# Kernel tuning notes

Measured on AMD Instinct MI355X. Metric: run time of the kernel, lower is better.

## Reference

```python
import jax, jax.numpy as jnp
import numpy as np

NUM_HEADS = 8
CUTOFF = 10.0


def layer_norm(x, g, b):
    m = x.mean(-1, keepdims=True)
    v = x.var(-1, keepdims=True)
    return (x - m) * jax.lax.rsqrt(v + 1e-5) * g + b


def mha(h, mask, Wq, Wk, Wv, Wo):
    # masked multi-head self-attention over the edge set; mask: [E,E] bool
    E, D = h.shape
    hd = D // NUM_HEADS
    q = (h @ Wq).reshape(E, NUM_HEADS, hd)
    k = (h @ Wk).reshape(E, NUM_HEADS, hd)
    v = (h @ Wv).reshape(E, NUM_HEADS, hd)
    s = jnp.einsum('ihd,jhd->hij', q, k) / jnp.sqrt(jnp.asarray(hd, h.dtype))
    s = jnp.where(mask[None], s, jnp.asarray(-1e9, h.dtype))
    p = jax.nn.softmax(s, axis=-1)  # [H,E,E]
    out = jnp.einsum('hij,jhd->ihd', p, v).reshape(E, D)
    return out @ Wo, p.mean(0)


def setup_inputs() -> dict:
    D, L, R, E, N, NB = 128, 3, 64, 3072, 1024, 16
    key = jax.random.key(0)
    ks = jax.random.split(key, 32)
    f32 = jnp.float32

    def w(i, shape, scale):
        return (jax.random.normal(ks[i], shape) * scale).astype(f32)

    s = 1.0 / np.sqrt(D)
    return {
        'edge_features': w(0, (E, D), 1.0),
        'edge_coords': w(1, (E, 3), 1.0),
        'edge_index': jax.random.randint(ks[2], (2, E), 0, N),
        'node_coords': w(3, (N, 3), 5.0),  # spread so distances span [0, cutoff]
        'block_ids': jax.random.randint(ks[4], (N,), 0, NB),
        'Wq_a': w(5, (L, D, D), s), 'Wk_a': w(6, (L, D, D), s),
        'Wv_a': w(7, (L, D, D), s), 'Wo_a': w(8, (L, D, D), s),
        'Wq_e': w(9, (L, D, D), s), 'Wk_e': w(10, (L, D, D), s),
        'Wv_e': w(11, (L, D, D), s), 'Wo_e': w(12, (L, D, D), s),
        'W1': w(13, (L, D, 4 * D), s), 'b1': jnp.zeros((L, 4 * D), f32),
        'W2': w(14, (L, 4 * D, D), 1.0 / np.sqrt(4 * D)), 'b2': jnp.zeros((L, D), f32),
        'ln1_g': jnp.ones((L, D), f32), 'ln1_b': jnp.zeros((L, D), f32),
        'ln2_g': jnp.ones((L, D), f32), 'ln2_b': jnp.zeros((L, D), f32),
        'ln3_g': jnp.ones((L, D), f32), 'ln3_b': jnp.zeros((L, D), f32),
        'Wrbf': w(15, (L, R, D), 1.0 / np.sqrt(R)),
        'Wc': w(16, (L, D), s), 'bc': jnp.zeros((L,), f32),
    }


def reference(edge_features, edge_coords, edge_index, node_coords, block_ids,
              Wq_a, Wk_a, Wv_a, Wo_a, Wq_e, Wk_e, Wv_e, Wo_e,
              W1, b1, W2, b2, ln1_g, ln1_b, ln2_g, ln2_b, ln3_g, ln3_b,
              Wrbf, Wc, bc):
    E = edge_features.shape[0]
    src, dst = edge_index[0], edge_index[1]
    bs, bd = block_ids[src], block_ids[dst]

    # intra-block mask: both endpoint blocks match between the two edges
    intra = (bs[:, None] == bs[None, :]) & (bd[:, None] == bd[None, :])
    # inter-block mask: edges that share a node but cross blocks
    share = ((src[:, None] == src[None, :]) | (src[:, None] == dst[None, :]) |
             (dst[:, None] == src[None, :]) | (dst[:, None] == dst[None, :]))
    inter = share & ~intra
    eye = jnp.eye(E, dtype=bool)
    intra = intra | eye
    inter = inter | eye

    # radial basis embedding of edge length with cosine cutoff
    R = Wrbf.shape[1]
    d = jnp.linalg.norm(node_coords[dst] - node_coords[src], axis=-1)  # [E]
    centers = jnp.linspace(0.0, CUTOFF, R).astype(edge_features.dtype)
    width = CUTOFF / R
    fc = 0.5 * (jnp.cos(jnp.pi * jnp.clip(d / CUTOFF, 0.0, 1.0)) + 1.0)
    rbf = jnp.exp(-(((d[:, None] - centers[None, :]) / width) ** 2)) * fc[:, None]

    h, x = edge_features, edge_coords
    L = Wq_a.shape[0]
    for l in range(L):
        h = h + rbf @ Wrbf[l]
        a, p_intra = mha(h, intra, Wq_a[l], Wk_a[l], Wv_a[l], Wo_a[l])
        h = layer_norm(h + a, ln1_g[l], ln1_b[l])
        e, _ = mha(h, inter, Wq_e[l], Wk_e[l], Wv_e[l], Wo_e[l])
        h = layer_norm(h + e, ln2_g[l], ln2_b[l])
        f = jax.nn.silu(h @ W1[l] + b1[l]) @ W2[l] + b2[l]
        h = layer_norm(h + f, ln3_g[l], ln3_b[l])
        # equivariant coordinate update (linear combination of equivariant vecs)
        gate = jnp.tanh(h @ Wc[l] + bc[l])[:, None]  # [E,1]
        x = x + gate * (x - p_intra @ x)
    return h, x
```

## Files before the change

### kernel.cpp

```cpp
#include <hip/hip_runtime.h>
#include <hip/hip_bf16.h>

typedef unsigned short u16;
typedef unsigned long long u64;
typedef __attribute__((ext_vector_type(4))) float f32x4;
typedef __attribute__((ext_vector_type(8))) short bf16x8;

#define NE 3072
#define DM 128
#define NH 8
#define HD 16
#define NL 3
#define NR 64
#define FF 512
#define CUT 10.0f
#define CAP 96
#define GRID 192
#define BR 16
#define NCLS 256

#define PK_QKV_A 0
#define PK_WO_A  49152
#define PK_QKV_E 65536
#define PK_WO_E  114688
#define PK_W1    131072
#define PK_W2    196608
#define PK_WRBF  262144
#define PK_LAYER 270336

__device__ __forceinline__ short f2b(float f) {
    union { __hip_bfloat16 b; short s; } u;
    u.b = __float2bfloat16(f);
    return u.s;
}
__device__ __forceinline__ void ast64(u64* p, u64 v) {
    __hip_atomic_store(p, v, __ATOMIC_RELAXED, __HIP_MEMORY_SCOPE_AGENT);
}
__device__ __forceinline__ void astf(float* p, float v) {
    __hip_atomic_store(p, v, __ATOMIC_RELAXED, __HIP_MEMORY_SCOPE_AGENT);
}
__device__ __forceinline__ float bfx(u64 v, int i) {
    return __uint_as_float(((unsigned)(v >> (16 * i)) & 0xFFFFu) << 16);
}

template <int KT, int S>
__device__ __forceinline__ f32x4 tileAb(const short* As, const short* Bt, int l) {
    f32x4 acc = {0.f, 0.f, 0.f, 0.f};
#pragma unroll
    for (int kt = 0; kt < KT; kt++) {
        bf16x8 av = *(const bf16x8*)(As + (l & 15) * S + kt * 32 + 8 * (l >> 4));
        bf16x8 bv = *(const bf16x8*)(Bt + kt * 512 + l * 8);
        acc = __builtin_amdgcn_mfma_f32_16x16x32_bf16(av, bv, acc, 0, 0, 0);
    }
    return acc;
}

__device__ __forceinline__ void gbar(int* cnt, int target) {
    __syncthreads();
    if (threadIdx.x == 0) {
        __hip_atomic_fetch_add(cnt, 1, __ATOMIC_RELEASE, __HIP_MEMORY_SCOPE_AGENT);
        while (__hip_atomic_load(cnt, __ATOMIC_RELAXED, __HIP_MEMORY_SCOPE_AGENT) < target)
            __builtin_amdgcn_s_sleep(2);
        asm volatile("" ::: "memory");
    }
    __syncthreads();
}

struct WSrc { const float* W[11]; };

__global__ __launch_bounds__(256)
void pack_w(WSrc ws, short* __restrict__ dst) {
    int gid = blockIdx.x * 256 + threadIdx.x;
    if (gid >= NL * PK_LAYER) return;
    int layer = gid / PK_LAYER, e = gid % PK_LAYER;
    int kind, off, K, N;
    if (e < 49152)       { kind = e / 16384;            off = e % 16384;      K = 128; N = 128; }
    else if (e < 65536)  { kind = 3;                    off = e - 49152;      K = 128; N = 128; }
    else if (e < 114688) { kind = 4 + (e - 65536) / 16384; off = (e - 65536) % 16384; K = 128; N = 128; }
    else if (e < 131072) { kind = 7;                    off = e - 114688;     K = 128; N = 128; }
    else if (e < 196608) { kind = 8;                    off = e - 131072;     K = 128; N = 512; }
    else if (e < 262144) { kind = 9;                    off = e - 196608;     K = 512; N = 128; }
    else                 { kind = 10;                   off = e - 262144;     K = 64;  N = 128; }
    int i = off & 7, lane = (off >> 3) & 63, ft = off >> 9;
    int KT = K >> 5;
    int kt = ft % KT, nt = ft / KT;
    int n = nt * 16 + (lane & 15);
    int k = kt * 32 + 8 * (lane >> 4) + i;
    const float* W = ws.W[kind] + (size_t)layer * K * N;
    dst[gid] = f2b(W[k * N + n]);
}

__global__ void zero_hist(int* hist, int* barcnt) {
    hist[threadIdx.x] = 0;
    if (threadIdx.x == 0) *barcnt = 0;
}

__global__ __launch_bounds__(256)
void k_meta(const int* __restrict__ eidx, const int* __restrict__ bids,
            int4* __restrict__ meta, int* __restrict__ key, int* __restrict__ hist) {
    int e = blockIdx.x * 256 + threadIdx.x;
    if (e >= NE) return;
    int s = eidx[e], d = eidx[NE + e];
    int bs = bids[s], bd = bids[d];
    meta[e] = make_int4(s, d, bs, bd);
    int kk = bs * 16 + bd;
    key[e] = kk;
    atomicAdd(&hist[kk], 1);
}

__global__ __launch_bounds__(256)
void k_scan(const int* __restrict__ hist, int* __restrict__ cls_start,
            int* __restrict__ fill) {
    __shared__ int sh[NCLS];
    int t = threadIdx.x;
    sh[t] = hist[t];
    __syncthreads();
    for (int off = 1; off < NCLS; off <<= 1) {
        int v = (t >= off) ? sh[t - off] : 0;
        __syncthreads();
        sh[t] += v;
        __syncthreads();
    }
    cls_start[t + 1] = sh[t];
    if (t == 0) cls_start[0] = 0;
    fill[t] = sh[t] - hist[t];
}

__global__ __launch_bounds__(256)
void k_scatter(const int* __restrict__ key, int* __restrict__ fill,
               int* __restrict__ perm) {
    int e = blockIdx.x * 256 + threadIdx.x;
    if (e >= NE) return;
    int pos = atomicAdd(&fill[key[e]], 1);
    perm[pos] = e;
}

__global__ __launch_bounds__(64)
void prep2(const float* __restrict__ ef, const float* __restrict__ ec,
           const float* __restrict__ nc, const int* __restrict__ perm,
           const int4* __restrict__ metaO, int4* __restrict__ meta2,
           float* __restrict__ h, float* __restrict__ xv, float* __restrict__ rbf) {
    int p = blockIdx.x, lane = threadIdx.x;
    int e = perm[p];
    int4 me = metaO[e];
    if (lane == 0) meta2[p] = me;
    h[p * DM + lane]      = ef[e * DM + lane];
    h[p * DM + 64 + lane] = ef[e * DM + 64 + lane];
    if (lane < 4) xv[p * 4 + lane] = (lane < 3) ? ec[e * 3 + lane] : 0.f;
    float dx = nc[me.y * 3 + 0] - nc[me.x * 3 + 0];
    float dy = nc[me.y * 3 + 1] - nc[me.x * 3 + 1];
    float dz = nc[me.y * 3 + 2] - nc[me.x * 3 + 2];
    float dist = sqrtf(dx * dx + dy * dy + dz * dz);
    float t = fminf(fmaxf(dist / CUT, 0.f), 1.f);
    float fc = 0.5f * (cosf(3.14159265358979f * t) + 1.f);
    float width = CUT / NR;
    float center = (CUT * lane) / (NR - 1);
    float u = (dist - center) / width;
    rbf[p * NR + lane] = expf(-u * u) * fc;
}

__global__ __launch_bounds__(64)
void build_lists(const int4* __restrict__ meta2,
                 u16* __restrict__ idx_e, int* __restrict__ cnt_e) {
    __shared__ int ce;
    __shared__ u16 be[CAP];
    int i = blockIdx.x, lane = threadIdx.x;
    if (lane == 0) ce = 0;
    __syncthreads();
    int4 mi = meta2[i];
    for (int j = lane; j < NE; j += 64) {
        int4 mj = meta2[j];
        bool intra_b = (mi.z == mj.z) && (mi.w == mj.w);
        bool share = (mi.x == mj.x) || (mi.x == mj.y) ||
                     (mi.y == mj.x) || (mi.y == mj.y);
        bool oke = (share && !intra_b) || (i == j);
        if (oke) { int p = atomicAdd(&ce, 1); if (p < CAP) be[p] = (u16)j; }
    }
    __syncthreads();
    int ne_ = min(ce, CAP);
    if (lane == 0) cnt_e[i] = ne_;
    for (int p = lane; p < ne_; p += 64) idx_e[i * CAP + p] = be[p];
}

__device__ __forceinline__ void attn_intra(
    const short (&qsb)[BR][136], const u64* __restrict__ kvaL,
    const float* __restrict__ xr, const int4* __restrict__ meta2,
    const int* __restrict__ cls_start,
    short (&ob)[BR][136], float (&pxs)[NH][BR][3],
    int m0, int w, int l)
{
    int rowl = l >> 2, sub = l & 3, row = m0 + rowl;
    const u64* q64 = reinterpret_cast<const u64*>(&qsb[rowl][w * HD]);
    u64 qc[4];
#pragma unroll
    for (int t = 0; t < 4; t++) qc[t] = q64[t];
    int4 mr = meta2[row];
    int c = mr.z * 16 + mr.w;
    int nb0 = cls_start[c], nb1 = cls_start[c + 1];

    float m = -1e30f, li = 0.f;
    float acc[HD + 3];
#pragma unroll
    for (int d = 0; d < HD + 3; d++) acc[d] = 0.f;

    for (int p2 = nb0 + sub; p2 < nb1; p2 += 4) {
        const u64* kb = kvaL + ((size_t)w * NE + p2) * 8;
        u64 kc[4], vc[4];
#pragma unroll
        for (int t = 0; t < 4; t++) { kc[t] = kb[t]; vc[t] = kb[4 + t]; }
        float x0 = xr[p2 * 4], x1 = xr[p2 * 4 + 1], x2 = xr[p2 * 4 + 2];
        float s = 0.f;
#pragma unroll
        for (int t = 0; t < 4; t++)
#pragma unroll
            for (int i = 0; i < 4; i++) s += bfx(qc[t], i) * bfx(kc[t], i);
        s *= 0.25f;
        if (s > m) {
            float cr = __expf(m - s);
            m = s; li *= cr;
#pragma unroll
            for (int d = 0; d < HD + 3; d++) acc[d] *= cr;
        }
        float pw = __expf(s - m);
        li += pw;
#pragma unroll
        for (int t = 0; t < 4; t++)
#pragma unroll
            for (int i = 0; i < 4; i++) acc[t * 4 + i] += pw * bfx(vc[t], i);
        acc[HD] += pw * x0; acc[HD + 1] += pw * x1; acc[HD + 2] += pw * x2;
    }

    float mA = fmaxf(m, __shfl_xor(m, 1));
    mA = fmaxf(mA, __shfl_xor(mA, 2));
    float cf = __expf(m - mA);
    li *= cf;
#pragma unroll
    for (int d = 0; d < HD + 3; d++) acc[d] *= cf;
#pragma unroll
    for (int off = 1; off <= 2; off <<= 1) {
        li += __shfl_xor(li, off);
#pragma unroll
        for (int d = 0; d < HD + 3; d++) acc[d] += __shfl_xor(acc[d], off);
    }
    if (sub == 0) {
        float inv = 1.f / li;
#pragma unroll
        for (int d = 0; d < HD; d += 2) {
            unsigned loq = (u16)f2b(acc[d] * inv);
            unsigned hiq = (u16)f2b(acc[d + 1] * inv);
            *reinterpret_cast<unsigned*>(&ob[rowl][w * HD + d]) = loq | (hiq << 16);
        }
        pxs[w][rowl][0] = acc[HD] * inv;
        pxs[w][rowl][1] = acc[HD + 1] * inv;
        pxs[w][rowl][2] = acc[HD + 2] * inv;
    }
}

__device__ __forceinline__ void attn_inter(
    const short (&qsb)[BR][136], const u64* __restrict__ kveL,
    const u16* __restrict__ idx, const int* __restrict__ cnt,
    short (&ob)[BR][136], int m0, int w, int l)
{
    int rowl = l >> 2, sub = l & 3, row = m0 + rowl;
    const u64* q64 = reinterpret_cast<const u64*>(&qsb[rowl][w * HD]);
    u64 qc[4];
#pragma unroll
    for (int t = 0; t < 4; t++) qc[t] = q64[t];
    const u64* kvh = kveL + (size_t)w * NE * 8;
    int n = cnt[row];
    float m = -1e30f, li = 0.f;
    float acc[HD];
#pragma unroll
    for (int d = 0; d < HD; d++) acc[d] = 0.f;

    for (int p = sub; p < n; p += 4) {
        int j = idx[row * CAP + p];
        const u64* kb = kvh + (size_t)j * 8;
        u64 kc[4], vc[4];
#pragma unroll
        for (int t = 0; t < 4; t++) { kc[t] = kb[t]; vc[t] = kb[4 + t]; }
        float s = 0.f;
#pragma unroll
        for (int t = 0; t < 4; t++)
#pragma unroll
            for (int i = 0; i < 4; i++) s += bfx(qc[t], i) * bfx(kc[t], i);
        s *= 0.25f;
        if (s > m) {
            float cr = __expf(m - s);
            m = s; li *= cr;
#pragma unroll
            for (int d = 0; d < HD; d++) acc[d] *= cr;
        }
        float pw = __expf(s - m);
        li += pw;
#pragma unroll
        for (int t = 0; t < 4; t++)
#pragma unroll
            for (int i = 0; i < 4; i++) acc[t * 4 + i] += pw * bfx(vc[t], i);
    }

    float mA = fmaxf(m, __shfl_xor(m, 1));
    mA = fmaxf(mA, __shfl_xor(mA, 2));
    float cf = __expf(m - mA);
    li *= cf;
#pragma unroll
    for (int d = 0; d < HD; d++) acc[d] *= cf;
#pragma unroll
    for (int off = 1; off <= 2; off <<= 1) {
        li += __shfl_xor(li, off);
#pragma unroll
        for (int d = 0; d < HD; d++) acc[d] += __shfl_xor(acc[d], off);
    }
    if (sub == 0) {
        float inv = 1.f / li;
#pragma unroll
        for (int d = 0; d < HD; d += 2) {
            unsigned loq = (u16)f2b(acc[d] * inv);
            unsigned hiq = (u16)f2b(acc[d + 1] * inv);
            *reinterpret_cast<unsigned*>(&ob[rowl][w * HD + d]) = loq | (hiq << 16);
        }
    }
}

__device__ __forceinline__ void ln_rows(float (&zs)[BR][132], float (&hF)[BR][132],
                                        short* hB, const float* g, const float* b,
                                        int w, int l) {
#pragma unroll
    for (int rr = 0; rr < 2; rr++) {
        int r = 2 * w + rr;
        float z0 = zs[r][l], z1 = zs[r][64 + l];
        float s = z0 + z1;
#pragma unroll
        for (int off = 32; off; off >>= 1) s += __shfl_xor(s, off);
        float mean = s * (1.f / DM);
        float d0 = z0 - mean, d1 = z1 - mean;
        float vs = d0 * d0 + d1 * d1;
#pragma unroll
        for (int off = 32; off; off >>= 1) vs += __shfl_xor(vs, off);
        float inv = rsqrtf(vs * (1.f / DM) + 1e-5f);
        float h0 = d0 * inv * g[l] + b[l];
        float h1 = d1 * inv * g[64 + l] + b[64 + l];
        hF[r][l] = h0; hF[r][64 + l] = h1;
        hB[r * 136 + l] = f2b(h0);
        hB[r * 136 + 64 + l] = f2b(h1);
    }
}

__global__ __launch_bounds__(512, 4)
void mega_kernel(const float* __restrict__ h_init, const float* __restrict__ rbf_g,
                 const int4* __restrict__ meta2, const int* __restrict__ cls_start,
                 const int* __restrict__ perm,
                 const u16* __restrict__ idx_e, const int* __restrict__ cnt_e,
                 const short* __restrict__ pk,
                 const float* __restrict__ b1g, const float* __restrict__ b2g,
                 const float* __restrict__ ln1g, const float* __restrict__ ln1b,
                 const float* __restrict__ ln2g, const float* __restrict__ ln2b,
                 const float* __restrict__ ln3g, const float* __restrict__ ln3b,
                 const float* __restrict__ Wcg, const float* __restrict__ bcg,
                 short* __restrict__ kva, short* __restrict__ kve,
                 float* __restrict__ xv, int* __restrict__ barcnt,
                 float* __restrict__ outp)
{
    __shared__ float hL[BR][132];
    __shared__ float hn[BR][132];
    __shared__ float zs[BR][132];
    __shared__ short qsb[BR][136];
    __shared__ short hb[BR][136];
    __shared__ short hnb[BR][136];
    __shared__ short ob[BR][136];
    __shared__ short rbfb[BR][72];
    __shared__ short ub[BR][520];
    __shared__ float pxs[NH][BR][3];

    int tid = threadIdx.x, w = tid >> 6, l = tid & 63;
    int m0 = blockIdx.x * BR;
    int R4 = 4 * (l >> 4), c0 = l & 15;

    for (int i = tid; i < BR * 128; i += 512) hL[i >> 7][i & 127] = h_init[m0 * DM + i];
    for (int i = tid; i < BR * 64; i += 512) rbfb[i >> 6][i & 63] = f2b(rbf_g[m0 * NR + i]);
    __syncthreads();

    int ph = 0;
    for (int lay = 0; lay < NL; lay++) {
        const short* Lb = pk + (size_t)lay * PK_LAYER;
        const float* xr = xv + (size_t)lay * NE * 4;
        float* xw2 = xv + (size_t)(lay + 1) * NE * 4;
        u64* kvaL = reinterpret_cast<u64*>(kva) + (size_t)lay * NH * NE * 8;
        u64* kveL = reinterpret_cast<u64*>(kve) + (size_t)lay * NH * NE * 8;
        bool last = (lay == NL - 1);

        {
            f32x4 acc = tileAb<2, 72>(&rbfb[0][0], Lb + PK_WRBF + w * 1024, l);
#pragma unroll
            for (int r = 0; r < 4; r++) {
                float z = acc[r] + hL[R4 + r][w * 16 + c0];
                hn[R4 + r][w * 16 + c0] = z;
                hnb[R4 + r][w * 16 + c0] = f2b(z);
            }
        }
        __syncthreads();
        {
            f32x4 aq = tileAb<4, 136>(&hnb[0][0], Lb + PK_QKV_A + 0 * 16384 + w * 2048, l);
#pragma unroll
            for (int r = 0; r < 4; r++) qsb[R4 + r][w * 16 + c0] = f2b(aq[r]);
            f32x4 ak = tileAb<4, 136>(&hnb[0][0], Lb + PK_QKV_A + 1 * 16384 + w * 2048, l);
            f32x4 av = tileAb<4, 136>(&hnb[0][0], Lb + PK_QKV_A + 2 * 16384 + w * 2048, l);
#pragma unroll
            for (int r = 0; r < 4; r++) {
                ub[R4 + r][w * 16 + c0] = f2b(ak[r]);
                ub[R4 + r][128 + w * 16 + c0] = f2b(av[r]);
            }
            __syncthreads();
            for (int u = tid; u < BR * 64; u += 512) {
                int r = u >> 6, rest = u & 63, hh = rest >> 3, j = rest & 7;
                int so = (j < 4) ? (hh * 16 + j * 4) : (128 + hh * 16 + (j - 4) * 4);
                u64 val = *reinterpret_cast<const u64*>(&ub[r][so]);
                ast64(kvaL + ((size_t)hh * NE + m0 + r) * 8 + j, val);
            }
        }
        gbar(barcnt, GRID * (++ph));

        attn_intra(qsb, kvaL, xr, meta2, cls_start, ob, pxs, m0, w, l);
        __syncthreads();
        {
            f32x4 d = tileAb<4, 136>(&ob[0][0], Lb + PK_WO_A + w * 2048, l);
#pragma unroll
            for (int r = 0; r < 4; r++)
                zs[R4 + r][w * 16 + c0] = d[r] + hn[R4 + r][w * 16 + c0];
        }
        __syncthreads();
        ln_rows(zs, hL, &hb[0][0], ln1g + lay * DM, ln1b + lay * DM, w, l);
        __syncthreads();

        {
            f32x4 aq = tileAb<4, 136>(&hb[0][0], Lb + PK_QKV_E + 0 * 16384 + w * 2048, l);
#pragma unroll
            for (int r = 0; r < 4; r++) qsb[R4 + r][w * 16 + c0] = f2b(aq[r]);
            f32x4 ak = tileAb<4, 136>(&hb[0][0], Lb + PK_QKV_E + 1 * 16384 + w * 2048, l);
            f32x4 av = tileAb<4, 136>(&hb[0][0], Lb + PK_QKV_E + 2 * 16384 + w * 2048, l);
#pragma unroll
            for (int r = 0; r < 4; r++) {
                ub[R4 + r][w * 16 + c0] = f2b(ak[r]);
                ub[R4 + r][128 + w * 16 + c0] = f2b(av[r]);
            }
            __syncthreads();
            for (int u = tid; u < BR * 64; u += 512) {
                int r = u >> 6, rest = u & 63, hh = rest >> 3, j = rest & 7;
                int so = (j < 4) ? (hh * 16 + j * 4) : (128 + hh * 16 + (j - 4) * 4);
                u64 val = *reinterpret_cast<const u64*>(&ub[r][so]);
                ast64(kveL + ((size_t)hh * NE + m0 + r) * 8 + j, val);
            }
        }
        gbar(barcnt, GRID * (++ph));

        attn_inter(qsb, kveL, idx_e, cnt_e, ob, m0, w, l);
        __syncthreads();
        {
            f32x4 d = tileAb<4, 136>(&ob[0][0], Lb + PK_WO_E + w * 2048, l);
#pragma unroll
            for (int r = 0; r < 4; r++)
                zs[R4 + r][w * 16 + c0] = d[r] + hL[R4 + r][w * 16 + c0];
        }
        __syncthreads();
        ln_rows(zs, hL, &hb[0][0], ln2g + lay * DM, ln2b + lay * DM, w, l);
        __syncthreads();

#pragma unroll
        for (int j = 0; j < 4; j++) {
            int nt = w * 4 + j;
            f32x4 acc = tileAb<4, 136>(&hb[0][0], Lb + PK_W1 + nt * 2048, l);
#pragma unroll
            for (int r = 0; r < 4; r++) {
                int col = nt * 16 + c0;
                float xvv = acc[r] + b1g[lay * FF + col];
                xvv = xvv / (1.f + __expf(-xvv));
                ub[R4 + r][col] = f2b(xvv);
            }
        }
        __syncthreads();
        {
            f32x4 acc = tileAb<16, 520>(&ub[0][0], Lb + PK_W2 + w * 8192, l);
#pragma unroll
            for (int r = 0; r < 4; r++)
                zs[R4 + r][w * 16 + c0] = acc[r] + b2g[lay * DM + w * 16 + c0]
                                        + hL[R4 + r][w * 16 + c0];
        }
        __syncthreads();
        {
            const float* g3 = ln3g + lay * DM;
            const float* b3 = ln3b + lay * DM;
            const float* Wcl = Wcg + lay * DM;
            float bc0 = bcg[lay];
#pragma unroll
            for (int rr = 0; rr < 2; rr++) {
                int r = 2 * w + rr, row = m0 + r;
                int orow = perm[row];
                float z0 = zs[r][l], z1 = zs[r][64 + l];
                float s = z0 + z1;
#pragma unroll
                for (int off = 32; off; off >>= 1) s += __shfl_xor(s, off);
                float mean = s * (1.f / DM);
                float d0 = z0 - mean, d1 = z1 - mean;
                float vsum = d0 * d0 + d1 * d1;
#pragma unroll
                for (int off = 32; off; off >>= 1) vsum += __shfl_xor(vsum, off);
                float inv = rsqrtf(vsum * (1.f / DM) + 1e-5f);
                float h0 = d0 * inv * g3[l] + b3[l];
                float h1 = d1 * inv * g3[64 + l] + b3[64 + l];
                hL[r][l] = h0; hL[r][64 + l] = h1;
                if (last) { outp[orow * DM + l] = h0; outp[orow * DM + 64 + l] = h1; }
                float dc = h0 * Wcl[l] + h1 * Wcl[64 + l];
#pragma unroll
                for (int off = 32; off; off >>= 1) dc += __shfl_xor(dc, off);
                float gate = tanhf(dc + bc0);
                if (l < 3) {
                    float pxm = 0.f;
#pragma unroll
                    for (int hh = 0; hh < NH; hh++) pxm += pxs[hh][r][l];
                    pxm *= 0.125f;
                    float xvv = xr[row * 4 + l];
                    float nx = xvv + gate * (xvv - pxm);
                    astf(xw2 + row * 4 + l, nx);
                    if (last) outp[NE * DM + orow * 3 + l] = nx;
                }
            }
        }
        __syncthreads();
    }
}

extern "C" void kernel_launch(void* const* d_in, const int* in_sizes, int n_in,
                              void* d_out, int out_size, void* d_ws, size_t ws_size,
                              hipStream_t stream) {
    const float* ef   = (const float*)d_in[0];
    const float* ec   = (const float*)d_in[1];
    const int*   eidx = (const int*)d_in[2];
    const float* nc   = (const float*)d_in[3];
    const int*   bids = (const int*)d_in[4];
    const float* b1   = (const float*)d_in[14];
    const float* b2   = (const float*)d_in[16];
    const float* ln1g = (const float*)d_in[17];
    const float* ln1b = (const float*)d_in[18];
    const float* ln2g = (const float*)d_in[19];
    const float* ln2b = (const float*)d_in[20];
    const float* ln3g = (const float*)d_in[21];
    const float* ln3b = (const float*)d_in[22];
    const float* Wc   = (const float*)d_in[24];
    const float* bc   = (const float*)d_in[25];
    float* out = (float*)d_out;

    char* w = (char*)d_ws;
    auto carve = [&](size_t bytes) { char* p = w; w += ((bytes + 255) / 256) * 256; return p; };
    int*   barcnt = (int*)carve(256);
    int*   hist   = (int*)carve(NCLS * 4);
    int*   csta   = (int*)carve((NCLS + 1) * 4);
    int*   fill   = (int*)carve(NCLS * 4);
    int*   key    = (int*)carve((size_t)NE * 4);
    int*   perm   = (int*)carve((size_t)NE * 4);
    int4*  metaO  = (int4*)carve((size_t)NE * 16);
    int4*  meta2  = (int4*)carve((size_t)NE * 16);
    float* xv     = (float*)carve((size_t)(NL + 1) * NE * 4 * 4);
    int*   cnt_e  = (int*)carve((size_t)NE * 4);
    u16*   idx_e  = (u16*)carve((size_t)NE * CAP * 2);
    float* rbf_g  = (float*)carve((size_t)NE * NR * 4);
    float* h_in   = (float*)carve((size_t)NE * DM * 4);
    short* kva    = (short*)carve((size_t)NL * NH * NE * 32 * 2);
    short* kve    = (short*)carve((size_t)NL * NH * NE * 32 * 2);
    short* pk     = (short*)carve((size_t)NL * PK_LAYER * 2);

    WSrc ws;
    ws.W[0] = (const float*)d_in[5];   ws.W[1] = (const float*)d_in[6];
    ws.W[2] = (const float*)d_in[7];   ws.W[3] = (const float*)d_in[8];
    ws.W[4] = (const float*)d_in[9];   ws.W[5] = (const float*)d_in[10];
    ws.W[6] = (const float*)d_in[11];  ws.W[7] = (const float*)d_in[12];
    ws.W[8] = (const float*)d_in[13];  ws.W[9] = (const float*)d_in[15];
    ws.W[10] = (const float*)d_in[23];
    pack_w<<<(NL * PK_LAYER + 255) / 256, 256, 0, stream>>>(ws, pk);

    zero_hist<<<1, 256, 0, stream>>>(hist, barcnt);
    k_meta<<<(NE + 255) / 256, 256, 0, stream>>>(eidx, bids, metaO, key, hist);
    k_scan<<<1, 256, 0, stream>>>(hist, csta, fill);
    k_scatter<<<(NE + 255) / 256, 256, 0, stream>>>(key, fill, perm);
    prep2<<<NE, 64, 0, stream>>>(ef, ec, nc, perm, metaO, meta2, h_in, xv, rbf_g);
    build_lists<<<NE, 64, 0, stream>>>(meta2, idx_e, cnt_e);

    mega_kernel<<<GRID, 512, 0, stream>>>(h_in, rbf_g, meta2, csta, perm,
                                          idx_e, cnt_e, pk,
                                          b1, b2, ln1g, ln1b, ln2g, ln2b, ln3g, ln3b,
                                          Wc, bc, kva, kve, xv, barcnt, out);
}
```

Measured before the change: 171.9 us.

## Fuse setup kernels into one persistent kernel and prefetch K/V in attention loops

Merges weight packing, histogram, scan, scatter, per-edge prep and neighbor-list construction into a single persistent setup kernel that uses grid-wide atomic barriers, replacing seven launches with two. The histogram scan becomes a wave-level shuffle scan, and edge metadata is stored with a 64-byte stride. Both attention loops now software-prefetch the next K/V row and coordinates before computing on the current one. The grid barriers assume all 384 blocks are co-resident, and the prefetch raises register pressure in the mega kernel.

```diff
diff --git a/kernel.cpp b/kernel.cpp
--- a/kernel.cpp
+++ b/kernel.cpp
@@ -18,6 +18,8 @@
 #define GRID 192
 #define BR 16
 #define NCLS 256
+#define SB 384
+#define ST 512
 
 #define PK_QKV_A 0
 #define PK_WO_A  49152
@@ -39,6 +41,9 @@
 __device__ __forceinline__ void astf(float* p, float v) {
     __hip_atomic_store(p, v, __ATOMIC_RELAXED, __HIP_MEMORY_SCOPE_AGENT);
 }
+__device__ __forceinline__ int aldi(const int* p) {
+    return __hip_atomic_load(p, __ATOMIC_RELAXED, __HIP_MEMORY_SCOPE_AGENT);
+}
 __device__ __forceinline__ float bfx(u64 v, int i) {
     return __uint_as_float(((unsigned)(v >> (16 * i)) & 0xFFFFu) << 16);
 }
@@ -68,123 +73,129 @@
 
 struct WSrc { const float* W[11]; };
 
-__global__ __launch_bounds__(256)
-void pack_w(WSrc ws, short* __restrict__ dst) {
-    int gid = blockIdx.x * 256 + threadIdx.x;
-    if (gid >= NL * PK_LAYER) return;
-    int layer = gid / PK_LAYER, e = gid % PK_LAYER;
-    int kind, off, K, N;
-    if (e < 49152)       { kind = e / 16384;            off = e % 16384;      K = 128; N = 128; }
-    else if (e < 65536)  { kind = 3;                    off = e - 49152;      K = 128; N = 128; }
-    else if (e < 114688) { kind = 4 + (e - 65536) / 16384; off = (e - 65536) % 16384; K = 128; N = 128; }
-    else if (e < 131072) { kind = 7;                    off = e - 114688;     K = 128; N = 128; }
-    else if (e < 196608) { kind = 8;                    off = e - 131072;     K = 128; N = 512; }
-    else if (e < 262144) { kind = 9;                    off = e - 196608;     K = 512; N = 128; }
-    else                 { kind = 10;                   off = e - 262144;     K = 64;  N = 128; }
-    int i = off & 7, lane = (off >> 3) & 63, ft = off >> 9;
-    int KT = K >> 5;
-    int kt = ft % KT, nt = ft / KT;
-    int n = nt * 16 + (lane & 15);
-    int k = kt * 32 + 8 * (lane >> 4) + i;
-    const float* W = ws.W[kind] + (size_t)layer * K * N;
-    dst[gid] = f2b(W[k * N + n]);
-}
-
-__global__ void zero_hist(int* hist, int* barcnt) {
-    hist[threadIdx.x] = 0;
-    if (threadIdx.x == 0) *barcnt = 0;
-}
-
-__global__ __launch_bounds__(256)
-void k_meta(const int* __restrict__ eidx, const int* __restrict__ bids,
-            int4* __restrict__ meta, int* __restrict__ key, int* __restrict__ hist) {
-    int e = blockIdx.x * 256 + threadIdx.x;
-    if (e >= NE) return;
-    int s = eidx[e], d = eidx[NE + e];
-    int bs = bids[s], bd = bids[d];
-    meta[e] = make_int4(s, d, bs, bd);
-    int kk = bs * 16 + bd;
-    key[e] = kk;
-    atomicAdd(&hist[kk], 1);
-}
-
-__global__ __launch_bounds__(256)
-void k_scan(const int* __restrict__ hist, int* __restrict__ cls_start,
-            int* __restrict__ fill) {
-    __shared__ int sh[NCLS];
+__global__ void zeroK(int* hist, int* barA, int* barM) {
     int t = threadIdx.x;
-    sh[t] = hist[t];
-    __syncthreads();
-    for (int off = 1; off < NCLS; off <<= 1) {
-        int v = (t >= off) ? sh[t - off] : 0;
-        __syncthreads();
-        sh[t] += v;
-        __syncthreads();
-    }
-    cls_start[t + 1] = sh[t];
-    if (t == 0) cls_start[0] = 0;
-    fill[t] = sh[t] - hist[t];
-}
-
-__global__ __launch_bounds__(256)
-void k_scatter(const int* __restrict__ key, int* __restrict__ fill,
-               int* __restrict__ perm) {
-    int e = blockIdx.x * 256 + threadIdx.x;
-    if (e >= NE) return;
-    int pos = atomicAdd(&fill[key[e]], 1);
-    perm[pos] = e;
-}
-
-__global__ __launch_bounds__(64)
-void prep2(const float* __restrict__ ef, const float* __restrict__ ec,
-           const float* __restrict__ nc, const int* __restrict__ perm,
-           const int4* __restrict__ metaO, int4* __restrict__ meta2,
-           float* __restrict__ h, float* __restrict__ xv, float* __restrict__ rbf) {
-    int p = blockIdx.x, lane = threadIdx.x;
-    int e = perm[p];
-    int4 me = metaO[e];
-    if (lane == 0) meta2[p] = me;
-    h[p * DM + lane]      = ef[e * DM + lane];
-    h[p * DM + 64 + lane] = ef[e * DM + 64 + lane];
-    if (lane < 4) xv[p * 4 + lane] = (lane < 3) ? ec[e * 3 + lane] : 0.f;
-    float dx = nc[me.y * 3 + 0] - nc[me.x * 3 + 0];
-    float dy = nc[me.y * 3 + 1] - nc[me.x * 3 + 1];
-    float dz = nc[me.y * 3 + 2] - nc[me.x * 3 + 2];
-    float dist = sqrtf(dx * dx + dy * dy + dz * dz);
-    float t = fminf(fmaxf(dist / CUT, 0.f), 1.f);
-    float fc = 0.5f * (cosf(3.14159265358979f * t) + 1.f);
-    float width = CUT / NR;
-    float center = (CUT * lane) / (NR - 1);
-    float u = (dist - center) / width;
-    rbf[p * NR + lane] = expf(-u * u) * fc;
-}
-
-__global__ __launch_bounds__(64)
-void build_lists(const int4* __restrict__ meta2,
-                 u16* __restrict__ idx_e, int* __restrict__ cnt_e) {
-    __shared__ int ce;
-    __shared__ u16 be[CAP];
-    int i = blockIdx.x, lane = threadIdx.x;
-    if (lane == 0) ce = 0;
-    __syncthreads();
-    int4 mi = meta2[i];
-    for (int j = lane; j < NE; j += 64) {
-        int4 mj = meta2[j];
-        bool intra_b = (mi.z == mj.z) && (mi.w == mj.w);
-        bool share = (mi.x == mj.x) || (mi.x == mj.y) ||
-                     (mi.y == mj.x) || (mi.y == mj.y);
-        bool oke = (share && !intra_b) || (i == j);
-        if (oke) { int p = atomicAdd(&ce, 1); if (p < CAP) be[p] = (u16)j; }
-    }
-    __syncthreads();
-    int ne_ = min(ce, CAP);
-    if (lane == 0) cnt_e[i] = ne_;
-    for (int p = lane; p < ne_; p += 64) idx_e[i * CAP + p] = be[p];
+    if (t < NCLS) hist[t] = 0;
+    if (t == 300) *barA = 0;
+    if (t == 301) *barM = 0;
+}
+
+__global__ __launch_bounds__(ST)
+void setup_kernel(const int* __restrict__ eidx, const int* __restrict__ bids,
+                  const float* __restrict__ ef, const float* __restrict__ ec,
+                  const float* __restrict__ nc, WSrc ws, short* __restrict__ pkd,
+                  int* __restrict__ key, int* __restrict__ hist,
+                  int* __restrict__ cls_start, int* __restrict__ fill,
+                  int* __restrict__ perm, int4* __restrict__ meta2p,
+                  float* __restrict__ h, float* __restrict__ xv,
+                  float* __restrict__ rbf,
+                  u16* __restrict__ idx_e, int* __restrict__ cnt_e,
+                  int* __restrict__ barA)
+{
+    __shared__ int ce[8];
+    __shared__ u16 be[8][CAP];
+    int tid = threadIdx.x, bid = blockIdx.x;
+    int gid = bid * ST + tid;
+    int w = tid >> 6, l = tid & 63;
+    int i = bid * 8 + w;
+
+    if (gid < NE) {
+        int s = eidx[gid], d = eidx[NE + gid];
+        int kk = bids[s] * 16 + bids[d];
+        key[gid] = kk;
+        atomicAdd(&hist[kk], 1);
+    }
+    for (int g = gid; g < NL * PK_LAYER; g += SB * ST) {
+        int layer = g / PK_LAYER, e = g % PK_LAYER;
+        int kind, off, K, N;
+        if (e < 49152)       { kind = e / 16384;            off = e % 16384;      K = 128; N = 128; }
+        else if (e < 65536)  { kind = 3;                    off = e - 49152;      K = 128; N = 128; }
+        else if (e < 114688) { kind = 4 + (e - 65536) / 16384; off = (e - 65536) % 16384; K = 128; N = 128; }
+        else if (e < 131072) { kind = 7;                    off = e - 114688;     K = 128; N = 128; }
+        else if (e < 196608) { kind = 8;                    off = e - 131072;     K = 128; N = 512; }
+        else if (e < 262144) { kind = 9;                    off = e - 196608;     K = 512; N = 128; }
+        else                 { kind = 10;                   off = e - 262144;     K = 64;  N = 128; }
+        int ii = off & 7, lane = (off >> 3) & 63, ft = off >> 9;
+        int KT = K >> 5;
+        int kt = ft % KT, nt = ft / KT;
+        int n = nt * 16 + (lane & 15);
+        int k = kt * 32 + 8 * (lane >> 4) + ii;
+        const float* W = ws.W[kind] + (size_t)layer * K * N;
+        pkd[g] = f2b(W[k * N + n]);
+    }
+    gbar(barA, SB);
+
+    if (bid == 0 && tid < 64) {
+        int b0 = hist[4 * tid], b1 = hist[4 * tid + 1],
+            b2 = hist[4 * tid + 2], b3 = hist[4 * tid + 3];
+        int c0 = b0, c1 = c0 + b1, c2 = c1 + b2, c3 = c2 + b3;
+        int S = c3;
+#pragma unroll
+        for (int off = 1; off < 64; off <<= 1) {
+            int v = __shfl_up(S, off);
+            if (tid >= off) S += v;
+        }
+        int base = S - c3;
+        cls_start[4 * tid + 1] = base + c0;
+        cls_start[4 * tid + 2] = base + c1;
+        cls_start[4 * tid + 3] = base + c2;
+        cls_start[4 * tid + 4] = base + c3;
+        if (tid == 0) cls_start[0] = 0;
+        fill[4 * tid]     = base;
+        fill[4 * tid + 1] = base + c0;
+        fill[4 * tid + 2] = base + c1;
+        fill[4 * tid + 3] = base + c2;
+    }
+    gbar(barA, 2 * SB);
+
+    if (gid < NE) {
+        int pos = atomicAdd(&fill[key[gid]], 1);
+        perm[pos] = gid;
+    }
+    gbar(barA, 3 * SB);
+
+    {
+        int e = aldi(perm + i);
+        int s = eidx[e], d = eidx[NE + e];
+        if (l == 0) meta2p[i * 4] = make_int4(s, d, bids[s], bids[d]);
+        h[i * DM + l]      = ef[e * DM + l];
+        h[i * DM + 64 + l] = ef[e * DM + 64 + l];
+        if (l < 4) xv[i * 4 + l] = (l < 3) ? ec[e * 3 + l] : 0.f;
+        float dx = nc[d * 3 + 0] - nc[s * 3 + 0];
+        float dy = nc[d * 3 + 1] - nc[s * 3 + 1];
+        float dz = nc[d * 3 + 2] - nc[s * 3 + 2];
+        float dist = sqrtf(dx * dx + dy * dy + dz * dz);
+        float t = fminf(fmaxf(dist / CUT, 0.f), 1.f);
+        float fc = 0.5f * (cosf(3.14159265358979f * t) + 1.f);
+        float width = CUT / NR;
+        float center = (CUT * l) / (NR - 1);
+        float u = (dist - center) / width;
+        rbf[i * NR + l] = expf(-u * u) * fc;
+    }
+    gbar(barA, 4 * SB);
+
+    {
+        if (l == 0) ce[w] = 0;
+        __builtin_amdgcn_wave_barrier();
+        int4 mi = meta2p[i * 4];
+        for (int j = l; j < NE; j += 64) {
+            int4 mj = meta2p[j * 4];
+            bool intra_b = (mi.z == mj.z) && (mi.w == mj.w);
+            bool share = (mi.x == mj.x) || (mi.x == mj.y) ||
+                         (mi.y == mj.x) || (mi.y == mj.y);
+            bool oke = (share && !intra_b) || (i == j);
+            if (oke) { int p = atomicAdd(&ce[w], 1); if (p < CAP) be[w][p] = (u16)j; }
+        }
+        __builtin_amdgcn_wave_barrier();
+        int ne_ = min(ce[w], CAP);
+        if (l == 0) cnt_e[i] = ne_;
+        for (int p = l; p < ne_; p += 64) idx_e[i * CAP + p] = be[w][p];
+    }
 }
 
 __device__ __forceinline__ void attn_intra(
     const short (&qsb)[BR][136], const u64* __restrict__ kvaL,
-    const float* __restrict__ xr, const int4* __restrict__ meta2,
+    const float* __restrict__ xr, const int4* __restrict__ meta2p,
     const int* __restrict__ cls_start,
     short (&ob)[BR][136], float (&pxs)[NH][BR][3],
     int m0, int w, int l)
@@ -194,7 +205,7 @@
     u64 qc[4];
 #pragma unroll
     for (int t = 0; t < 4; t++) qc[t] = q64[t];
-    int4 mr = meta2[row];
+    int4 mr = meta2p[row * 4];
     int c = mr.z * 16 + mr.w;
     int nb0 = cls_start[c], nb1 = cls_start[c + 1];
 
@@ -203,12 +214,25 @@
 #pragma unroll
     for (int d = 0; d < HD + 3; d++) acc[d] = 0.f;
 
-    for (int p2 = nb0 + sub; p2 < nb1; p2 += 4) {
-        const u64* kb = kvaL + ((size_t)w * NE + p2) * 8;
-        u64 kc[4], vc[4];
-#pragma unroll
-        for (int t = 0; t < 4; t++) { kc[t] = kb[t]; vc[t] = kb[4 + t]; }
-        float x0 = xr[p2 * 4], x1 = xr[p2 * 4 + 1], x2 = xr[p2 * 4 + 2];
+    int p2 = nb0 + sub;
+    bool have = p2 < nb1;
+    int pc = have ? p2 : nb0;
+    const u64* kb = kvaL + ((size_t)w * NE + pc) * 8;
+    u64 kc[4], vc[4];
+#pragma unroll
+    for (int t = 0; t < 4; t++) { kc[t] = kb[t]; vc[t] = kb[4 + t]; }
+    float x0 = xr[pc * 4], x1 = xr[pc * 4 + 1], x2 = xr[pc * 4 + 2];
+
+    while (have) {
+        int pn = p2 + 4;
+        bool haveN = pn < nb1;
+        int pl = haveN ? pn : nb0;
+        const u64* kbn = kvaL + ((size_t)w * NE + pl) * 8;
+        u64 nk[4], nv[4];
+#pragma unroll
+        for (int t = 0; t < 4; t++) { nk[t] = kbn[t]; nv[t] = kbn[4 + t]; }
+        float nx0 = xr[pl * 4], nx1 = xr[pl * 4 + 1], nx2 = xr[pl * 4 + 2];
+
         float s = 0.f;
 #pragma unroll
         for (int t = 0; t < 4; t++)
@@ -228,6 +252,11 @@
 #pragma unroll
             for (int i = 0; i < 4; i++) acc[t * 4 + i] += pw * bfx(vc[t], i);
         acc[HD] += pw * x0; acc[HD + 1] += pw * x1; acc[HD + 2] += pw * x2;
+
+        p2 = pn; have = haveN;
+#pragma unroll
+        for (int t = 0; t < 4; t++) { kc[t] = nk[t]; vc[t] = nv[t]; }
+        x0 = nx0; x1 = nx1; x2 = nx2;
     }
 
     float mA = fmaxf(m, __shfl_xor(m, 1));
@@ -273,12 +302,23 @@
 #pragma unroll
     for (int d = 0; d < HD; d++) acc[d] = 0.f;
 
-    for (int p = sub; p < n; p += 4) {
-        int j = idx[row * CAP + p];
-        const u64* kb = kvh + (size_t)j * 8;
-        u64 kc[4], vc[4];
-#pragma unroll
-        for (int t = 0; t < 4; t++) { kc[t] = kb[t]; vc[t] = kb[4 + t]; }
+    int p = sub;
+    bool have = p < n;
+    int jc = have ? (int)idx[row * CAP + p] : 0;
+    const u64* kb = kvh + (size_t)jc * 8;
+    u64 kc[4], vc[4];
+#pragma unroll
+    for (int t = 0; t < 4; t++) { kc[t] = kb[t]; vc[t] = kb[4 + t]; }
+
+    while (have) {
+        int pn = p + 4;
+        bool haveN = pn < n;
+        int jn = haveN ? (int)idx[row * CAP + pn] : 0;
+        const u64* kbn = kvh + (size_t)jn * 8;
+        u64 nk[4], nv[4];
+#pragma unroll
+        for (int t = 0; t < 4; t++) { nk[t] = kbn[t]; nv[t] = kbn[4 + t]; }
+
         float s = 0.f;
 #pragma unroll
         for (int t = 0; t < 4; t++)
@@ -297,6 +337,10 @@
         for (int t = 0; t < 4; t++)
 #pragma unroll
             for (int i = 0; i < 4; i++) acc[t * 4 + i] += pw * bfx(vc[t], i);
+
+        p = pn; have = haveN;
+#pragma unroll
+        for (int t = 0; t < 4; t++) { kc[t] = nk[t]; vc[t] = nv[t]; }
     }
 
     float mA = fmaxf(m, __shfl_xor(m, 1));
@@ -348,7 +392,7 @@
 
 __global__ __launch_bounds__(512, 4)
 void mega_kernel(const float* __restrict__ h_init, const float* __restrict__ rbf_g,
-                 const int4* __restrict__ meta2, const int* __restrict__ cls_start,
+                 const int4* __restrict__ meta2p, const int* __restrict__ cls_start,
                  const int* __restrict__ perm,
                  const u16* __restrict__ idx_e, const int* __restrict__ cnt_e,
                  const short* __restrict__ pk,
@@ -420,7 +464,7 @@
         }
         gbar(barcnt, GRID * (++ph));
 
-        attn_intra(qsb, kvaL, xr, meta2, cls_start, ob, pxs, m0, w, l);
+        attn_intra(qsb, kvaL, xr, meta2p, cls_start, ob, pxs, m0, w, l);
         __syncthreads();
         {
             f32x4 d = tileAb<4, 136>(&ob[0][0], Lb + PK_WO_A + w * 2048, l);
@@ -551,14 +595,14 @@
 
     char* w = (char*)d_ws;
     auto carve = [&](size_t bytes) { char* p = w; w += ((bytes + 255) / 256) * 256; return p; };
-    int*   barcnt = (int*)carve(256);
+    int*   barM   = (int*)carve(256);
+    int*   barA   = (int*)carve(256);
     int*   hist   = (int*)carve(NCLS * 4);
     int*   csta   = (int*)carve((NCLS + 1) * 4);
     int*   fill   = (int*)carve(NCLS * 4);
     int*   key    = (int*)carve((size_t)NE * 4);
     int*   perm   = (int*)carve((size_t)NE * 4);
-    int4*  metaO  = (int4*)carve((size_t)NE * 16);
-    int4*  meta2  = (int4*)carve((size_t)NE * 16);
+    int4*  meta2p = (int4*)carve((size_t)NE * 64);
     float* xv     = (float*)carve((size_t)(NL + 1) * NE * 4 * 4);
     int*   cnt_e  = (int*)carve((size_t)NE * 4);
     u16*   idx_e  = (u16*)carve((size_t)NE * CAP * 2);
@@ -575,17 +619,13 @@
     ws.W[6] = (const float*)d_in[11];  ws.W[7] = (const float*)d_in[12];
     ws.W[8] = (const float*)d_in[13];  ws.W[9] = (const float*)d_in[15];
     ws.W[10] = (const float*)d_in[23];
-    pack_w<<<(NL * PK_LAYER + 255) / 256, 256, 0, stream>>>(ws, pk);
-
-    zero_hist<<<1, 256, 0, stream>>>(hist, barcnt);
-    k_meta<<<(NE + 255) / 256, 256, 0, stream>>>(eidx, bids, metaO, key, hist);
-    k_scan<<<1, 256, 0, stream>>>(hist, csta, fill);
-    k_scatter<<<(NE + 255) / 256, 256, 0, stream>>>(key, fill, perm);
-    prep2<<<NE, 64, 0, stream>>>(ef, ec, nc, perm, metaO, meta2, h_in, xv, rbf_g);
-    build_lists<<<NE, 64, 0, stream>>>(meta2, idx_e, cnt_e);
-
-    mega_kernel<<<GRID, 512, 0, stream>>>(h_in, rbf_g, meta2, csta, perm,
+
+    zeroK<<<1, 512, 0, stream>>>(hist, barA, barM);
+    setup_kernel<<<SB, ST, 0, stream>>>(eidx, bids, ef, ec, nc, ws, pk,
+                                        key, hist, csta, fill, perm, meta2p,
+                                        h_in, xv, rbf_g, idx_e, cnt_e, barA);
+    mega_kernel<<<GRID, 512, 0, stream>>>(h_in, rbf_g, meta2p, csta, perm,
                                           idx_e, cnt_e, pk,
                                           b1, b2, ln1g, ln1b, ln2g, ln2b, ln3g, ln3b,
-                                          Wc, bc, kva, kve, xv, barcnt, out);
-}
+                                          Wc, bc, kva, kve, xv, barM, out);
+}
```

Measured after the change: 238.4 us. +38.7%, slower.
